# Performance work log

Measured on AMD Instinct MI355X. Metric: run time of the kernel, lower is better.

Reference implementation:

```python
import jax, jax.numpy as jnp
import numpy as np

B, T, U, NOUT = 64, 512, 256, 4


def lstm(x, W, Uh, b):
    """Keras-style LSTM. x: [B,T,F]. Returns (seq [B,T,U], last [B,U]).
    Gate order i, f, g(candidate), o; sigmoid recurrent activation, tanh activation."""
    xz = jnp.einsum('btf,fg->btg', x, W) + b  # precompute input projections [B,T,4U]

    def step(carry, xz_t):
        h, c = carry
        z = xz_t + h @ Uh
        i, f, g, o = jnp.split(z, 4, axis=-1)
        i = jax.nn.sigmoid(i)
        f = jax.nn.sigmoid(f)
        g = jnp.tanh(g)
        o = jax.nn.sigmoid(o)
        c = f * c + i * g
        h = o * jnp.tanh(c)
        return (h, c), h

    h0 = jnp.zeros((x.shape[0], Uh.shape[0]), x.dtype)
    (h_last, _), hs = jax.lax.scan(step, (h0, h0), jnp.swapaxes(xz, 0, 1))
    return jnp.swapaxes(hs, 0, 1), h_last


def setup_inputs() -> dict:
    key = jax.random.key(0)
    ks = jax.random.split(key, 7)
    s_in = 1.0 / np.sqrt(U)
    return {
        'x': jax.random.normal(ks[0], (B, T, U), jnp.float32),
        'Wr': jax.random.normal(ks[1], (U, 4 * U), jnp.float32) * s_in,
        'Ur': jax.random.normal(ks[2], (U, 4 * U), jnp.float32) * s_in,
        'br': jnp.zeros((4 * U,), jnp.float32),
        'Wn': jax.random.normal(ks[3], (U, 4 * U), jnp.float32) * s_in,
        'Un': jax.random.normal(ks[4], (U, 4 * U), jnp.float32) * s_in,
        'bn': jnp.zeros((4 * U,), jnp.float32),
        'Wd': jax.random.normal(ks[5], (T * U, NOUT), jnp.float32) * (1.0 / np.sqrt(T * U)),
        'bd': jnp.zeros((NOUT,), jnp.float32),
    }


def reference(x, Wr, Ur, br, Wn, Un, bn, Wd, bd):
    # n_hidden = 3, inference (training=False): noise/dropout are identity.
    # Layer 0: shared return-sequences LSTM, no residual.
    h0, _ = lstm(x, Wr, Ur, br)                      # [B,T,U]
    # Layer 1: SAME shared LSTM weights, residual add.
    h1, _ = lstm(h0, Wr, Ur, br)
    h1 = h1 + h0                                     # [B,T,U]
    # Layer 2 (last): non-returning LSTM; residual Add broadcasts [B,U] + [B,T,U].
    _, h2 = lstm(h1, Wn, Un, bn)                     # [B,U]
    y = h2[:, None, :] + h1                          # [B,T,U]
    y = y.reshape(y.shape[0], -1)                    # flatten -> [B, T*U]
    return y @ Wd + bd                               # [B, NOUT]
```

## Files before the change

### kernel.cpp

```cpp
#include <hip/hip_runtime.h>
#include <hip/hip_fp16.h>
#include <cstddef>
#include <cstdint>

#define U_DIM 256
#define G_DIM 1024
#define T_DIM 512
#define B_DIM 64
#define TC    64
#define NCHUNK (T_DIM / TC)
#define NSLOT  (NCHUNK + 2)
#define BHID   (B_DIM * U_DIM)
#define NPART  8

#define NG_TOT 32
#define NG_REG 23
#define NG_LDS 9

typedef _Float16 half2v __attribute__((ext_vector_type(2)));
typedef _Float16 f16x8  __attribute__((ext_vector_type(8)));
typedef float    f32x4  __attribute__((ext_vector_type(4)));

__device__ __forceinline__ float fsig(float x) {
    return 1.0f / (1.0f + __expf(-x));
}
__device__ __forceinline__ float ftanh(float x) {
    return 2.0f * fsig(2.0f * x) - 1.0f;
}

#define PIN4(v) asm("" : "+v"(v.x), "+v"(v.y), "+v"(v.z), "+v"(v.w))

__global__ __launch_bounds__(256)
void pack_w(const float* __restrict__ U, uint4* __restrict__ P)
{
    const int idx = blockIdx.x * 256 + threadIdx.x;
    const int g = idx >> 10;
    const int n = idx & 1023;
    uint vals[4];
    #pragma unroll
    for (int j = 0; j < 4; ++j) {
        const int k = g * 8 + j * 2;
        const __half a = __float2half_rn(U[(size_t)k * G_DIM + n]);
        const __half b = __float2half_rn(U[(size_t)(k + 1) * G_DIM + n]);
        const unsigned short ua = __builtin_bit_cast(unsigned short, a);
        const unsigned short ub = __builtin_bit_cast(unsigned short, b);
        vals[j] = (uint)ua | ((uint)ub << 16);
    }
    P[idx] = make_uint4(vals[0], vals[1], vals[2], vals[3]);
}

__global__ __launch_bounds__(256)
void pack_x(const float* __restrict__ x, __half* __restrict__ xh)
{
    const size_t i = ((size_t)blockIdx.x * 256 + threadIdx.x) * 8;
    const float4 a = *(const float4*)(x + i);
    const float4 b = *(const float4*)(x + i + 4);
    ushort4 o0, o1;
    o0.x = __builtin_bit_cast(unsigned short, __float2half_rn(a.x));
    o0.y = __builtin_bit_cast(unsigned short, __float2half_rn(a.y));
    o0.z = __builtin_bit_cast(unsigned short, __float2half_rn(a.z));
    o0.w = __builtin_bit_cast(unsigned short, __float2half_rn(a.w));
    o1.x = __builtin_bit_cast(unsigned short, __float2half_rn(b.x));
    o1.y = __builtin_bit_cast(unsigned short, __float2half_rn(b.y));
    o1.z = __builtin_bit_cast(unsigned short, __float2half_rn(b.z));
    o1.w = __builtin_bit_cast(unsigned short, __float2half_rn(b.w));
    *(ushort4*)(xh + i) = o0;
    *(ushort4*)(xh + i + 4) = o1;
}

__device__ __forceinline__ float mac8(float acc, uint4 w, uint4 h)
{
#if __has_builtin(__builtin_amdgcn_fdot2)
    acc = __builtin_amdgcn_fdot2(__builtin_bit_cast(half2v, h.x),
                                 __builtin_bit_cast(half2v, w.x), acc, false);
    acc = __builtin_amdgcn_fdot2(__builtin_bit_cast(half2v, h.y),
                                 __builtin_bit_cast(half2v, w.y), acc, false);
    acc = __builtin_amdgcn_fdot2(__builtin_bit_cast(half2v, h.z),
                                 __builtin_bit_cast(half2v, w.z), acc, false);
    acc = __builtin_amdgcn_fdot2(__builtin_bit_cast(half2v, h.w),
                                 __builtin_bit_cast(half2v, w.w), acc, false);
#else
    const uint wv[4] = {w.x, w.y, w.z, w.w};
    const uint hv[4] = {h.x, h.y, h.z, h.w};
    #pragma unroll
    for (int j = 0; j < 4; ++j) {
        const __half2 wp = __builtin_bit_cast(__half2, wv[j]);
        const __half2 hp = __builtin_bit_cast(__half2, hv[j]);
        acc += __half2float(hp.x) * __half2float(wp.x);
        acc += __half2float(hp.y) * __half2float(wp.y);
    }
#endif
    return acc;
}

__global__
__attribute__((amdgpu_flat_work_group_size(512, 512)))
__attribute__((amdgpu_waves_per_eu(2, 2)))
void lstm_pipe(int slot,
               const __half* __restrict__ xzAll,
               const uint4* __restrict__ Pr, const uint4* __restrict__ Pn,
               __half* __restrict__ h0, __half* __restrict__ h1,
               float* __restrict__ hsAll, float* __restrict__ csAll)
{
    const int layer = blockIdx.x >> 6;
    const int b     = blockIdx.x & 63;
    const int c     = slot - layer;
    if ((unsigned)c >= (unsigned)NCHUNK) return;
    const int t0 = c * TC;

    const uint4* __restrict__ P = (layer < 2) ? Pr : Pn;
    const __half* __restrict__ xzb =
        xzAll + (size_t)layer * (B_DIM * TC * G_DIM) + (size_t)b * TC * G_DIM;
    const __half* __restrict__ resb =
        (layer == 1) ? (h0 + (size_t)(b * T_DIM + t0) * U_DIM) : nullptr;
    __half* __restrict__ outb =
        (layer == 0) ? (h0 + (size_t)(b * T_DIM + t0) * U_DIM)
      : (layer == 1) ? (h1 + (size_t)(b * T_DIM + t0) * U_DIM) : nullptr;
    float* __restrict__ hstate = hsAll + (size_t)layer * BHID + b * U_DIM;
    float* __restrict__ cstate = csAll + (size_t)layer * BHID + b * U_DIM;

    const int t = threadIdx.x;
    const int n0 = t;
    const int n1 = t + 512;

    __shared__ __align__(16) uint hq[U_DIM / 2];
    __shared__ float csh[U_DIM];
    __shared__ float zsh[G_DIM];
    __shared__ uint4 wlds[NG_LDS][G_DIM];

    uint4 wA[NG_REG], wB[NG_REG];
    #pragma unroll
    for (int g = 0; g < NG_REG; ++g) {
        wA[g] = P[(size_t)g * G_DIM + n0];
        wB[g] = P[(size_t)g * G_DIM + n1];
    }
    #pragma unroll
    for (int g = 0; g < NG_REG; ++g) { PIN4(wA[g]); PIN4(wB[g]); }
    #pragma unroll
    for (int g = 0; g < NG_LDS; ++g) {
        wlds[g][n0] = P[(size_t)(NG_REG + g) * G_DIM + n0];
        wlds[g][n1] = P[(size_t)(NG_REG + g) * G_DIM + n1];
    }

    if (t < U_DIM) {
        float hv, cv;
        if (c == 0) { hv = 0.0f; cv = 0.0f; }
        else        { hv = hstate[t]; cv = cstate[t]; }
        csh[t] = cv;
        ((__half*)hq)[t] = __float2half_rn(hv);
    }
    __syncthreads();

    float cur0 = __half2float(xzb[n0]);
    float cur1 = __half2float(xzb[n1]);
    float resv = (resb && t < U_DIM) ? __half2float(resb[t]) : 0.0f;

    for (int tl = 0; tl < TC; ++tl) {
        float acc0 = cur0;
        float acc1 = cur1;

        const int tn = (tl + 1 < TC) ? (tl + 1) : (TC - 1);
        cur0 = __half2float(xzb[(size_t)tn * G_DIM + n0]);
        cur1 = __half2float(xzb[(size_t)tn * G_DIM + n1]);
        const float resn = (resb && t < U_DIM)
                         ? __half2float(resb[(size_t)tn * U_DIM + t]) : 0.0f;

        const uint4* __restrict__ hp = (const uint4*)hq;

        #pragma unroll
        for (int g = 0; g < NG_REG; ++g) {
            const uint4 h4 = hp[g];
            acc0 = mac8(acc0, wA[g], h4);
            acc1 = mac8(acc1, wB[g], h4);
        }
        #pragma unroll
        for (int g = 0; g < NG_LDS; ++g) {
            const uint4 h4 = hp[NG_REG + g];
            acc0 = mac8(acc0, wlds[g][n0], h4);
            acc1 = mac8(acc1, wlds[g][n1], h4);
        }

        zsh[n0] = fsig(acc0);
        zsh[n1] = (t < U_DIM) ? ftanh(acc1) : fsig(acc1);
        __syncthreads();

        if (t < U_DIM) {
            const float iv = zsh[t];
            const float fv = zsh[t + 256];
            const float gv = zsh[t + 512];
            const float ov = zsh[t + 768];
            const float cc = fv * csh[t] + iv * gv;
            const float hh = ov * ftanh(cc);
            csh[t] = cc;
            ((__half*)hq)[t] = __float2half_rn(hh);
            if (outb) outb[(size_t)tl * U_DIM + t] = __float2half_rn(hh + resv);
        }
        resv = resn;
        __syncthreads();
    }

    if (t < U_DIM) {
        hstate[t] = __half2float(((const __half*)hq)[t]);
        cstate[t] = csh[t];
    }
}

__global__ __launch_bounds__(256)
void gemm3_mfma(int slot,
                const __half* __restrict__ xh,
                const __half* __restrict__ h0, const __half* __restrict__ h1,
                const uint4* __restrict__ PWr, const uint4* __restrict__ PWn,
                const float* __restrict__ br, const float* __restrict__ bn,
                __half* __restrict__ xzAll)
{
    const int z = blockIdx.z;
    const int c = slot - z;
    if ((unsigned)c >= (unsigned)NCHUNK) return;
    const int t0 = c * TC;

    const __half* __restrict__ A = (z == 0) ? xh : ((z == 1) ? h0 : h1);
    const uint4*  __restrict__ PW = (z < 2) ? PWr : PWn;
    const float*  __restrict__ bias = (z < 2) ? br : bn;
    __half* __restrict__ out = xzAll + (size_t)z * (B_DIM * TC * G_DIM);

    const int tid = threadIdx.x;
    const int w = tid >> 6;
    const int l = tid & 63;

    const int bm = blockIdx.y * 64;
    const int bn_ = blockIdx.x * 64;
    const int col = bn_ + w * 16 + (l & 15);
    const int krow = l >> 4;

    const __half* arow[4];
    #pragma unroll
    for (int rt = 0; rt < 4; ++rt) {
        const int m = bm + rt * 16 + (l & 15);
        const int b = m >> 6;
        const int tl = m & (TC - 1);
        arow[rt] = A + (size_t)(b * T_DIM + t0 + tl) * U_DIM + krow * 8;
    }

    f32x4 acc[4] = {{0,0,0,0},{0,0,0,0},{0,0,0,0},{0,0,0,0}};

    #pragma unroll
    for (int kt = 0; kt < 8; ++kt) {
        const uint4 bfrag = PW[(size_t)(4 * kt + krow) * G_DIM + col];
        #pragma unroll
        for (int rt = 0; rt < 4; ++rt) {
            const uint4 afrag = *(const uint4*)(arow[rt] + kt * 32);
            acc[rt] = __builtin_amdgcn_mfma_f32_16x16x32_f16(
                __builtin_bit_cast(f16x8, afrag), __builtin_bit_cast(f16x8, bfrag),
                acc[rt], 0, 0, 0);
        }
    }

    const float bv = bias[col];
    #pragma unroll
    for (int rt = 0; rt < 4; ++rt) {
        #pragma unroll
        for (int r = 0; r < 4; ++r) {
            const int m = bm + rt * 16 + 4 * (l >> 4) + r;
            const int b = m >> 6;
            const int tl = m & (TC - 1);
            out[(size_t)(b * TC + tl) * G_DIM + col] = __float2half_rn(acc[rt][r] + bv);
        }
    }
}

__global__ __launch_bounds__(256)
void final_partial(const __half* __restrict__ h1, const float* __restrict__ h2,
                   const float* __restrict__ Wd, float* __restrict__ partials)
{
    const int b = blockIdx.x;
    const int p = blockIdx.y;
    const int tid = threadIdx.x;
    const int JTOT = T_DIM * U_DIM;
    const int JPART = JTOT / NPART;

    const __half* hb = h1 + (size_t)b * JTOT;
    const float* h2b = h2 + (size_t)b * U_DIM;

    float a0 = 0.f, a1 = 0.f, a2 = 0.f, a3 = 0.f;

    for (int j = p * JPART + tid * 8; j < (p + 1) * JPART; j += 256 * 8) {
        const uint4 hv = *(const uint4*)(hb + j);
        const int m = j & (U_DIM - 1);
        const float4 s0 = *(const float4*)(h2b + m);
        const float4 s1 = *(const float4*)(h2b + m + 4);
        float v[8];
        {
            const __half2 p0 = __builtin_bit_cast(__half2, hv.x);
            const __half2 p1 = __builtin_bit_cast(__half2, hv.y);
            const __half2 p2 = __builtin_bit_cast(__half2, hv.z);
            const __half2 p3 = __builtin_bit_cast(__half2, hv.w);
            v[0] = __half2float(p0.x) + s0.x;
            v[1] = __half2float(p0.y) + s0.y;
            v[2] = __half2float(p1.x) + s0.z;
            v[3] = __half2float(p1.y) + s0.w;
            v[4] = __half2float(p2.x) + s1.x;
            v[5] = __half2float(p2.y) + s1.y;
            v[6] = __half2float(p3.x) + s1.z;
            v[7] = __half2float(p3.y) + s1.w;
        }
        #pragma unroll
        for (int u = 0; u < 8; ++u) {
            const float4 wv = *(const float4*)&Wd[(size_t)(j + u) * 4];
            a0 += v[u] * wv.x;
            a1 += v[u] * wv.y;
            a2 += v[u] * wv.z;
            a3 += v[u] * wv.w;
        }
    }

    __shared__ float red[256][4];
    red[tid][0] = a0; red[tid][1] = a1; red[tid][2] = a2; red[tid][3] = a3;
    __syncthreads();
    for (int s = 128; s > 0; s >>= 1) {
        if (tid < s) {
            #pragma unroll
            for (int o = 0; o < 4; ++o) red[tid][o] += red[tid + s][o];
        }
        __syncthreads();
    }
    if (tid < 4) partials[((size_t)b * NPART + p) * 4 + tid] = red[0][tid];
}

__global__ __launch_bounds__(256)
void final_reduce(const float* __restrict__ partials, const float* __restrict__ bd,
                  float* __restrict__ y)
{
    const int tid = threadIdx.x;
    const int b = tid >> 2;
    const int o = tid & 3;
    float s = bd[o];
    #pragma unroll
    for (int p = 0; p < NPART; ++p)
        s += partials[((size_t)b * NPART + p) * 4 + o];
    y[b * 4 + o] = s;
}

extern "C" void kernel_launch(void* const* d_in, const int* in_sizes, int n_in,
                              void* d_out, int out_size, void* d_ws, size_t ws_size,
                              hipStream_t stream)
{
    (void)in_sizes; (void)n_in; (void)out_size; (void)ws_size;

    const float* x  = (const float*)d_in[0];
    const float* Wr = (const float*)d_in[1];
    const float* Ur = (const float*)d_in[2];
    const float* br = (const float*)d_in[3];
    const float* Wn = (const float*)d_in[4];
    const float* Un = (const float*)d_in[5];
    const float* bn = (const float*)d_in[6];
    const float* Wd = (const float*)d_in[7];
    const float* bd = (const float*)d_in[8];
    float* y = (float*)d_out;

    char* wp = (char*)d_ws;
    uint4* Pr  = (uint4*)wp;                      wp += (size_t)NG_TOT * G_DIM * 16;
    uint4* Pn  = (uint4*)wp;                      wp += (size_t)NG_TOT * G_DIM * 16;
    uint4* PWr = (uint4*)wp;                      wp += (size_t)NG_TOT * G_DIM * 16;
    uint4* PWn = (uint4*)wp;                      wp += (size_t)NG_TOT * G_DIM * 16;
    float* hsAll = (float*)wp;                    wp += (size_t)3 * BHID * 4;
    float* csAll = (float*)wp;                    wp += (size_t)3 * BHID * 4;
    float* partials = (float*)wp;                 wp += (size_t)B_DIM * NPART * 4 * 4;
    __half* xzAll = (__half*)wp;                  wp += (size_t)3 * B_DIM * TC * G_DIM * 2;
    __half* h0 = (__half*)wp;                     wp += (size_t)B_DIM * T_DIM * U_DIM * 2;
    __half* h1 = (__half*)wp;                     wp += (size_t)B_DIM * T_DIM * U_DIM * 2;
    __half* xh = (__half*)wp;                     wp += (size_t)B_DIM * T_DIM * U_DIM * 2;

    pack_w<<<128, 256, 0, stream>>>(Ur, Pr);
    pack_w<<<128, 256, 0, stream>>>(Un, Pn);
    pack_w<<<128, 256, 0, stream>>>(Wr, PWr);
    pack_w<<<128, 256, 0, stream>>>(Wn, PWn);
    pack_x<<<(B_DIM * T_DIM * U_DIM) / (256 * 8), 256, 0, stream>>>(x, xh);

    dim3 ggrid(G_DIM / 64, (B_DIM * TC) / 64, 3);
    for (int slot = 0; slot < NSLOT; ++slot) {
        gemm3_mfma<<<ggrid, 256, 0, stream>>>(slot, xh, h0, h1, PWr, PWn,
                                              br, bn, xzAll);
        lstm_pipe<<<3 * B_DIM, 512, 0, stream>>>(slot, xzAll, Pr, Pn,
                                                 h0, h1, hsAll, csAll);
    }

    final_partial<<<dim3(B_DIM, NPART), 256, 0, stream>>>(h1, hsAll + 2 * BHID,
                                                          Wd, partials);
    final_reduce<<<1, 256, 0, stream>>>(partials, bd, y);
}
```

Before: 1.700 ms.

## Fuse chunked LSTM layers into one persistent cooperative kernel with flag sync

New measurement: 2.611 ms. +53.6%, slower.

```diff
diff --git a/kernel.cpp b/kernel.cpp
--- a/kernel.cpp
+++ b/kernel.cpp
@@ -7,10 +7,8 @@
 #define G_DIM 1024
 #define T_DIM 512
 #define B_DIM 64
-#define TC    64
+#define TC    32
 #define NCHUNK (T_DIM / TC)
-#define NSLOT  (NCHUNK + 2)
-#define BHID   (B_DIM * U_DIM)
 #define NPART  8
 
 #define NG_TOT 32
@@ -96,32 +94,36 @@
 __global__
 __attribute__((amdgpu_flat_work_group_size(512, 512)))
 __attribute__((amdgpu_waves_per_eu(2, 2)))
-void lstm_pipe(int slot,
-               const __half* __restrict__ xzAll,
-               const uint4* __restrict__ Pr, const uint4* __restrict__ Pn,
-               __half* __restrict__ h0, __half* __restrict__ h1,
-               float* __restrict__ hsAll, float* __restrict__ csAll)
+void lstm_persist(const __half* __restrict__ xh,
+                  const uint4* __restrict__ Pr, const uint4* __restrict__ Pn,
+                  const uint4* __restrict__ PWr, const uint4* __restrict__ PWn,
+                  const float* __restrict__ br, const float* __restrict__ bn,
+                  __half* __restrict__ h0, __half* __restrict__ h1,
+                  __half* __restrict__ xzAll, float* __restrict__ hs2,
+                  unsigned* __restrict__ flags)
 {
     const int layer = blockIdx.x >> 6;
     const int b     = blockIdx.x & 63;
-    const int c     = slot - layer;
-    if ((unsigned)c >= (unsigned)NCHUNK) return;
-    const int t0 = c * TC;
-
-    const uint4* __restrict__ P = (layer < 2) ? Pr : Pn;
-    const __half* __restrict__ xzb =
-        xzAll + (size_t)layer * (B_DIM * TC * G_DIM) + (size_t)b * TC * G_DIM;
-    const __half* __restrict__ resb =
-        (layer == 1) ? (h0 + (size_t)(b * T_DIM + t0) * U_DIM) : nullptr;
-    __half* __restrict__ outb =
-        (layer == 0) ? (h0 + (size_t)(b * T_DIM + t0) * U_DIM)
-      : (layer == 1) ? (h1 + (size_t)(b * T_DIM + t0) * U_DIM) : nullptr;
-    float* __restrict__ hstate = hsAll + (size_t)layer * BHID + b * U_DIM;
-    float* __restrict__ cstate = csAll + (size_t)layer * BHID + b * U_DIM;
-
     const int t = threadIdx.x;
+    const int w = t >> 6;
+    const int l = t & 63;
+    const int krow = l >> 4;
     const int n0 = t;
     const int n1 = t + 512;
+
+    const uint4* __restrict__ P    = (layer < 2) ? Pr : Pn;
+    const uint4* __restrict__ PW   = (layer < 2) ? PWr : PWn;
+    const float* __restrict__ bias = (layer < 2) ? br : bn;
+    const __half* __restrict__ src =
+        ((layer == 0) ? xh : (layer == 1) ? h0 : h1) + (size_t)b * T_DIM * U_DIM;
+    __half* __restrict__ outseq =
+        (layer == 0) ? (h0 + (size_t)b * T_DIM * U_DIM)
+      : (layer == 1) ? (h1 + (size_t)b * T_DIM * U_DIM) : nullptr;
+    const __half* __restrict__ resbase =
+        (layer == 1) ? (h0 + (size_t)b * T_DIM * U_DIM) : nullptr;
+    __half* __restrict__ xzb = xzAll + (size_t)(layer * B_DIM + b) * (TC * G_DIM);
+    unsigned* __restrict__ wflag = (layer > 0) ? (flags + (layer - 1) * B_DIM + b) : nullptr;
+    unsigned* __restrict__ pflag = (layer < 2) ? (flags + layer * B_DIM + b) : nullptr;
 
     __shared__ __align__(16) uint hq[U_DIM / 2];
     __shared__ float csh[U_DIM];
@@ -142,130 +144,108 @@
         wlds[g][n1] = P[(size_t)(NG_REG + g) * G_DIM + n1];
     }
 
-    if (t < U_DIM) {
-        float hv, cv;
-        if (c == 0) { hv = 0.0f; cv = 0.0f; }
-        else        { hv = hstate[t]; cv = cstate[t]; }
-        csh[t] = cv;
-        ((__half*)hq)[t] = __float2half_rn(hv);
-    }
+    if (t < U_DIM) { csh[t] = 0.0f; ((__half*)hq)[t] = __float2half_rn(0.0f); }
     __syncthreads();
 
-    float cur0 = __half2float(xzb[n0]);
-    float cur1 = __half2float(xzb[n1]);
-    float resv = (resb && t < U_DIM) ? __half2float(resb[t]) : 0.0f;
-
-    for (int tl = 0; tl < TC; ++tl) {
-        float acc0 = cur0;
-        float acc1 = cur1;
-
-        const int tn = (tl + 1 < TC) ? (tl + 1) : (TC - 1);
-        cur0 = __half2float(xzb[(size_t)tn * G_DIM + n0]);
-        cur1 = __half2float(xzb[(size_t)tn * G_DIM + n1]);
-        const float resn = (resb && t < U_DIM)
-                         ? __half2float(resb[(size_t)tn * U_DIM + t]) : 0.0f;
-
-        const uint4* __restrict__ hp = (const uint4*)hq;
+    for (int c = 0; c < NCHUNK; ++c) {
+        const int t0 = c * TC;
+
+        if (wflag) {
+            if (t == 0) {
+                while (__hip_atomic_load(wflag, __ATOMIC_ACQUIRE,
+                                         __HIP_MEMORY_SCOPE_AGENT) < (unsigned)(c + 1))
+                    __builtin_amdgcn_s_sleep(2);
+            }
+            __syncthreads();
+        }
 
         #pragma unroll
-        for (int g = 0; g < NG_REG; ++g) {
-            const uint4 h4 = hp[g];
-            acc0 = mac8(acc0, wA[g], h4);
-            acc1 = mac8(acc1, wB[g], h4);
-        }
-        #pragma unroll
-        for (int g = 0; g < NG_LDS; ++g) {
-            const uint4 h4 = hp[NG_REG + g];
-            acc0 = mac8(acc0, wlds[g][n0], h4);
-            acc1 = mac8(acc1, wlds[g][n1], h4);
-        }
-
-        zsh[n0] = fsig(acc0);
-        zsh[n1] = (t < U_DIM) ? ftanh(acc1) : fsig(acc1);
+        for (int ct = 0; ct < 8; ++ct) {
+            const int col = w * 128 + ct * 16 + (l & 15);
+            f32x4 acc0 = {0.f, 0.f, 0.f, 0.f};
+            f32x4 acc1 = {0.f, 0.f, 0.f, 0.f};
+            const __half* a0p = src + (size_t)(t0 + (l & 15)) * U_DIM + krow * 8;
+            const __half* a1p = a0p + 16 * U_DIM;
+            #pragma unroll
+            for (int kt = 0; kt < 8; ++kt) {
+                const uint4 bfrag = PW[(size_t)(4 * kt + krow) * G_DIM + col];
+                const uint4 a0 = *(const uint4*)(a0p + kt * 32);
+                const uint4 a1 = *(const uint4*)(a1p + kt * 32);
+                acc0 = __builtin_amdgcn_mfma_f32_16x16x32_f16(
+                    __builtin_bit_cast(f16x8, a0), __builtin_bit_cast(f16x8, bfrag),
+                    acc0, 0, 0, 0);
+                acc1 = __builtin_amdgcn_mfma_f32_16x16x32_f16(
+                    __builtin_bit_cast(f16x8, a1), __builtin_bit_cast(f16x8, bfrag),
+                    acc1, 0, 0, 0);
+            }
+            const float bv = bias[col];
+            #pragma unroll
+            for (int r = 0; r < 4; ++r) {
+                const int row0 = 4 * krow + r;
+                xzb[(size_t)row0 * G_DIM + col]        = __float2half_rn(acc0[r] + bv);
+                xzb[(size_t)(row0 + 16) * G_DIM + col] = __float2half_rn(acc1[r] + bv);
+            }
+        }
         __syncthreads();
 
-        if (t < U_DIM) {
-            const float iv = zsh[t];
-            const float fv = zsh[t + 256];
-            const float gv = zsh[t + 512];
-            const float ov = zsh[t + 768];
-            const float cc = fv * csh[t] + iv * gv;
-            const float hh = ov * ftanh(cc);
-            csh[t] = cc;
-            ((__half*)hq)[t] = __float2half_rn(hh);
-            if (outb) outb[(size_t)tl * U_DIM + t] = __float2half_rn(hh + resv);
-        }
-        resv = resn;
-        __syncthreads();
-    }
-
-    if (t < U_DIM) {
-        hstate[t] = __half2float(((const __half*)hq)[t]);
-        cstate[t] = csh[t];
-    }
-}
-
-__global__ __launch_bounds__(256)
-void gemm3_mfma(int slot,
-                const __half* __restrict__ xh,
-                const __half* __restrict__ h0, const __half* __restrict__ h1,
-                const uint4* __restrict__ PWr, const uint4* __restrict__ PWn,
-                const float* __restrict__ br, const float* __restrict__ bn,
-                __half* __restrict__ xzAll)
-{
-    const int z = blockIdx.z;
-    const int c = slot - z;
-    if ((unsigned)c >= (unsigned)NCHUNK) return;
-    const int t0 = c * TC;
-
-    const __half* __restrict__ A = (z == 0) ? xh : ((z == 1) ? h0 : h1);
-    const uint4*  __restrict__ PW = (z < 2) ? PWr : PWn;
-    const float*  __restrict__ bias = (z < 2) ? br : bn;
-    __half* __restrict__ out = xzAll + (size_t)z * (B_DIM * TC * G_DIM);
-
-    const int tid = threadIdx.x;
-    const int w = tid >> 6;
-    const int l = tid & 63;
-
-    const int bm = blockIdx.y * 64;
-    const int bn_ = blockIdx.x * 64;
-    const int col = bn_ + w * 16 + (l & 15);
-    const int krow = l >> 4;
-
-    const __half* arow[4];
-    #pragma unroll
-    for (int rt = 0; rt < 4; ++rt) {
-        const int m = bm + rt * 16 + (l & 15);
-        const int b = m >> 6;
-        const int tl = m & (TC - 1);
-        arow[rt] = A + (size_t)(b * T_DIM + t0 + tl) * U_DIM + krow * 8;
-    }
-
-    f32x4 acc[4] = {{0,0,0,0},{0,0,0,0},{0,0,0,0},{0,0,0,0}};
-
-    #pragma unroll
-    for (int kt = 0; kt < 8; ++kt) {
-        const uint4 bfrag = PW[(size_t)(4 * kt + krow) * G_DIM + col];
-        #pragma unroll
-        for (int rt = 0; rt < 4; ++rt) {
-            const uint4 afrag = *(const uint4*)(arow[rt] + kt * 32);
-            acc[rt] = __builtin_amdgcn_mfma_f32_16x16x32_f16(
-                __builtin_bit_cast(f16x8, afrag), __builtin_bit_cast(f16x8, bfrag),
-                acc[rt], 0, 0, 0);
-        }
-    }
-
-    const float bv = bias[col];
-    #pragma unroll
-    for (int rt = 0; rt < 4; ++rt) {
-        #pragma unroll
-        for (int r = 0; r < 4; ++r) {
-            const int m = bm + rt * 16 + 4 * (l >> 4) + r;
-            const int b = m >> 6;
-            const int tl = m & (TC - 1);
-            out[(size_t)(b * TC + tl) * G_DIM + col] = __float2half_rn(acc[rt][r] + bv);
-        }
-    }
+        const __half* __restrict__ resb = resbase ? (resbase + (size_t)t0 * U_DIM) : nullptr;
+        __half* __restrict__ outb = outseq ? (outseq + (size_t)t0 * U_DIM) : nullptr;
+
+        float cur0 = __half2float(xzb[n0]);
+        float cur1 = __half2float(xzb[n1]);
+        float resv = (resb && t < U_DIM) ? __half2float(resb[t]) : 0.0f;
+
+        for (int tl = 0; tl < TC; ++tl) {
+            float acc0 = cur0;
+            float acc1 = cur1;
+
+            const int tn = (tl + 1 < TC) ? (tl + 1) : (TC - 1);
+            cur0 = __half2float(xzb[(size_t)tn * G_DIM + n0]);
+            cur1 = __half2float(xzb[(size_t)tn * G_DIM + n1]);
+            const float resn = (resb && t < U_DIM)
+                             ? __half2float(resb[(size_t)tn * U_DIM + t]) : 0.0f;
+
+            const uint4* __restrict__ hp = (const uint4*)hq;
+
+            #pragma unroll
+            for (int g = 0; g < NG_REG; ++g) {
+                const uint4 h4 = hp[g];
+                acc0 = mac8(acc0, wA[g], h4);
+                acc1 = mac8(acc1, wB[g], h4);
+            }
+            #pragma unroll
+            for (int g = 0; g < NG_LDS; ++g) {
+                const uint4 h4 = hp[NG_REG + g];
+                acc0 = mac8(acc0, wlds[g][n0], h4);
+                acc1 = mac8(acc1, wlds[g][n1], h4);
+            }
+
+            zsh[n0] = fsig(acc0);
+            zsh[n1] = (t < U_DIM) ? ftanh(acc1) : fsig(acc1);
+            __syncthreads();
+
+            if (t < U_DIM) {
+                const float iv = zsh[t];
+                const float fv = zsh[t + 256];
+                const float gv = zsh[t + 512];
+                const float ov = zsh[t + 768];
+                const float cc = fv * csh[t] + iv * gv;
+                const float hh = ov * ftanh(cc);
+                csh[t] = cc;
+                ((__half*)hq)[t] = __float2half_rn(hh);
+                if (outb) outb[(size_t)tl * U_DIM + t] = __float2half_rn(hh + resv);
+            }
+            resv = resn;
+            __syncthreads();
+        }
+
+        if (pflag && t == 0)
+            __hip_atomic_store(pflag, (unsigned)(c + 1), __ATOMIC_RELEASE,
+                               __HIP_MEMORY_SCOPE_AGENT);
+    }
+
+    if (layer == 2 && t < U_DIM)
+        hs2[b * U_DIM + t] = __half2float(((const __half*)hq)[t]);
 }
 
 __global__ __launch_bounds__(256)
@@ -358,17 +338,18 @@
     float* y = (float*)d_out;
 
     char* wp = (char*)d_ws;
-    uint4* Pr  = (uint4*)wp;                      wp += (size_t)NG_TOT * G_DIM * 16;
-    uint4* Pn  = (uint4*)wp;                      wp += (size_t)NG_TOT * G_DIM * 16;
-    uint4* PWr = (uint4*)wp;                      wp += (size_t)NG_TOT * G_DIM * 16;
-    uint4* PWn = (uint4*)wp;                      wp += (size_t)NG_TOT * G_DIM * 16;
-    float* hsAll = (float*)wp;                    wp += (size_t)3 * BHID * 4;
-    float* csAll = (float*)wp;                    wp += (size_t)3 * BHID * 4;
-    float* partials = (float*)wp;                 wp += (size_t)B_DIM * NPART * 4 * 4;
-    __half* xzAll = (__half*)wp;                  wp += (size_t)3 * B_DIM * TC * G_DIM * 2;
-    __half* h0 = (__half*)wp;                     wp += (size_t)B_DIM * T_DIM * U_DIM * 2;
-    __half* h1 = (__half*)wp;                     wp += (size_t)B_DIM * T_DIM * U_DIM * 2;
-    __half* xh = (__half*)wp;                     wp += (size_t)B_DIM * T_DIM * U_DIM * 2;
+    uint4* Pr  = (uint4*)wp;  wp += (size_t)NG_TOT * G_DIM * 16;
+    uint4* Pn  = (uint4*)wp;  wp += (size_t)NG_TOT * G_DIM * 16;
+    uint4* PWr = (uint4*)wp;  wp += (size_t)NG_TOT * G_DIM * 16;
+    uint4* PWn = (uint4*)wp;  wp += (size_t)NG_TOT * G_DIM * 16;
+    float* hs2 = (float*)wp;  wp += (size_t)B_DIM * U_DIM * 4;
+    float* partials = (float*)wp;   wp += (size_t)B_DIM * NPART * 4 * 4;
+    unsigned* flags = (unsigned*)wp; wp += 2 * B_DIM * sizeof(unsigned);
+    wp = (char*)(((uintptr_t)wp + 255) & ~(uintptr_t)255);
+    __half* xzAll = (__half*)wp; wp += (size_t)3 * B_DIM * TC * G_DIM * 2;
+    __half* h0 = (__half*)wp;    wp += (size_t)B_DIM * T_DIM * U_DIM * 2;
+    __half* h1 = (__half*)wp;    wp += (size_t)B_DIM * T_DIM * U_DIM * 2;
+    __half* xh = (__half*)wp;    wp += (size_t)B_DIM * T_DIM * U_DIM * 2;
 
     pack_w<<<128, 256, 0, stream>>>(Ur, Pr);
     pack_w<<<128, 256, 0, stream>>>(Un, Pn);
@@ -376,15 +357,19 @@
     pack_w<<<128, 256, 0, stream>>>(Wn, PWn);
     pack_x<<<(B_DIM * T_DIM * U_DIM) / (256 * 8), 256, 0, stream>>>(x, xh);
 
-    dim3 ggrid(G_DIM / 64, (B_DIM * TC) / 64, 3);
-    for (int slot = 0; slot < NSLOT; ++slot) {
-        gemm3_mfma<<<ggrid, 256, 0, stream>>>(slot, xh, h0, h1, PWr, PWn,
-                                              br, bn, xzAll);
-        lstm_pipe<<<3 * B_DIM, 512, 0, stream>>>(slot, xzAll, Pr, Pn,
-                                                 h0, h1, hsAll, csAll);
-    }
-
-    final_partial<<<dim3(B_DIM, NPART), 256, 0, stream>>>(h1, hsAll + 2 * BHID,
-                                                          Wd, partials);
+    hipMemsetAsync(flags, 0, 2 * B_DIM * sizeof(unsigned), stream);
+
+    const __half* xh_c = xh;
+    const uint4 *Pr_c = Pr, *Pn_c = Pn, *PWr_c = PWr, *PWn_c = PWn;
+    const float *br_c = br, *bn_c = bn;
+    void* kargs[] = {
+        (void*)&xh_c, (void*)&Pr_c, (void*)&Pn_c, (void*)&PWr_c, (void*)&PWn_c,
+        (void*)&br_c, (void*)&bn_c, (void*)&h0, (void*)&h1,
+        (void*)&xzAll, (void*)&hs2, (void*)&flags
+    };
+    hipLaunchCooperativeKernel((void*)lstm_persist, dim3(3 * B_DIM), dim3(512),
+                               kargs, 0, stream);
+
+    final_partial<<<dim3(B_DIM, NPART), 256, 0, stream>>>(h1, hs2, Wd, partials);
     final_reduce<<<1, 256, 0, stream>>>(partials, bd, y);
 }
```
